# Kernel tuning notes

Hardware: AMD Instinct MI355X
Metric: run time of the kernel (lower is better)

## Reference

```python
import jax, jax.numpy as jnp
import numpy as np

FG_FRACTION = 0.5
FG_THRESH = 0.7
BG_HI = 0.5
BG_LO = 0.1
BATCHSIZE = 256
FG_ROIS = int(round(FG_FRACTION * BATCHSIZE))  # 128


def setup_inputs() -> dict:
    key = jax.random.key(0)
    k1, k2, k3 = jax.random.split(key, 3)
    N, K, C = 80000, 256, 81
    IMG = 800.0

    def make_boxes(k, n):
        ka, kb = jax.random.split(k)
        xy = jax.random.uniform(ka, (1, n, 2), dtype=jnp.float32) * (IMG - 136.0)
        wh = jax.random.uniform(kb, (1, n, 2), dtype=jnp.float32) * 128.0 + 8.0
        return jnp.concatenate([xy, xy + wh], axis=-1)  # valid x1<x2, y1<y2

    proposals = make_boxes(k1, N)          # (1, N, 4)
    gt_boxes = make_boxes(k2, K)           # (1, K, 4)
    cls = jax.random.randint(k3, (K,), 1, C)
    gt_labels = jax.nn.one_hot(cls, C, dtype=jnp.float32)[None]  # (1, K, C)
    return {"proposals": proposals, "gt_labels": gt_labels, "gt_boxes": gt_boxes}


def _iou(a, b):
    # a: (M,4), b: (K,4); keras_rcnn +1-pixel convention
    area_a = (a[:, 2] - a[:, 0] + 1.0) * (a[:, 3] - a[:, 1] + 1.0)
    area_b = (b[:, 2] - b[:, 0] + 1.0) * (b[:, 3] - b[:, 1] + 1.0)
    x1 = jnp.maximum(a[:, None, 0], b[None, :, 0])
    y1 = jnp.maximum(a[:, None, 1], b[None, :, 1])
    x2 = jnp.minimum(a[:, None, 2], b[None, :, 2])
    y2 = jnp.minimum(a[:, None, 3], b[None, :, 3])
    iw = jnp.maximum(x2 - x1 + 1.0, 0.0)
    ih = jnp.maximum(y2 - y1 + 1.0, 0.0)
    inter = iw * ih  # (M, K)
    return inter / (area_a[:, None] + area_b[None, :] - inter)


def _bbox_transform(ex, gt):
    ew = ex[:, 2] - ex[:, 0] + 1.0
    eh = ex[:, 3] - ex[:, 1] + 1.0
    ecx = ex[:, 0] + 0.5 * ew
    ecy = ex[:, 1] + 0.5 * eh
    gw = gt[:, 2] - gt[:, 0] + 1.0
    gh = gt[:, 3] - gt[:, 1] + 1.0
    gcx = gt[:, 0] + 0.5 * gw
    gcy = gt[:, 1] + 0.5 * gh
    return jnp.stack([(gcx - ecx) / ew, (gcy - ecy) / eh,
                      jnp.log(gw / ew), jnp.log(gh / eh)], axis=1)  # (B, 4)


def _forward(proposals, gt_labels, gt_boxes):
    all_rois = jnp.concatenate([proposals[0], gt_boxes[0]], axis=0)  # (M, 4)
    gt_b = gt_boxes[0]    # (K, 4)
    gt_l = gt_labels[0]   # (K, C)
    C = gt_l.shape[1]

    ov = _iou(all_rois, gt_b)               # (M, K)
    gt_assign = jnp.argmax(ov, axis=1)      # (M,)
    max_ov = jnp.max(ov, axis=1)            # (M,)

    fg_mask = max_ov >= FG_THRESH
    bg_mask = (max_ov < BG_HI) & (max_ov >= BG_LO)

    M = all_rois.shape[0]
    order = jnp.arange(M)
    # deterministic stand-in for random shuffle: candidates first, in index order
    fg_sorted = jnp.argsort(jnp.where(fg_mask, order, M + order))
    bg_sorted = jnp.argsort(jnp.where(bg_mask, order, M + order))
    num_fg = jnp.sum(fg_mask.astype(jnp.int32))
    fg_take = jnp.minimum(FG_ROIS, num_fg)

    pos = jnp.arange(BATCHSIZE)
    is_fg_slot = pos < fg_take
    keep = jnp.where(is_fg_slot,
                     fg_sorted[jnp.clip(pos, 0, M - 1)],
                     bg_sorted[jnp.clip(pos - fg_take, 0, M - 1)])  # (B,)

    rois = all_rois[keep]                    # (B, 4)
    labels = gt_l[gt_assign[keep]]           # (B, C)
    # set_label_background: bg slots -> one-hot class 0
    bg_onehot = jax.nn.one_hot(0, C, dtype=labels.dtype)
    labels = jnp.where(is_fg_slot[:, None], labels, bg_onehot[None, :])

    assigned_gt = gt_b[gt_assign[keep]]      # (B, 4)
    targets = _bbox_transform(rois, assigned_gt)  # (B, 4)

    # expand to N x 4K: only the argmax class (if > 0) gets nonzero targets
    clss = jnp.argmax(labels, axis=1)        # (B,)
    cls_oh = jnp.where((clss > 0)[:, None],
                       jax.nn.one_hot(clss, C, dtype=targets.dtype), 0.0)  # (B, C)
    bbox_targets = (cls_oh[:, :, None] * targets[:, None, :]).reshape(BATCHSIZE, 4 * C)

    return rois[None], labels[None], bbox_targets[None]


def reference(proposals, gt_labels, gt_boxes):
    return _forward(proposals, gt_labels, gt_boxes)
```

## Files before the change

kernel.cpp:

```cpp
#include <hip/hip_runtime.h>

#define FG_THRESH 0.7f
#define BG_HI 0.5f
#define BG_LO 0.1f
#define BATCH 256
#define FG_ROIS 128
#define KGT 256
#define CLS 81
#define NCHPAD2 1536
#define CPT2 3
#define NBIN 26
#define NSPAN 6

typedef unsigned long long ull;

__global__ __launch_bounds__(256) void k_iou(
    const float* __restrict__ proposals,
    const float* __restrict__ gt_boxes,
    int N, int M,
    int* __restrict__ gt_assign,
    ull* __restrict__ fgm,
    ull* __restrict__ bgm)
{
    __shared__ float4 gshE[KGT];
    __shared__ float garea[KGT];
    __shared__ ull pbx[4][NBIN], pby[4][NBIN];
    __shared__ ull intX[4][NBIN][NSPAN], intY[4][NBIN][NSPAN];

    int tid = threadIdx.x;
    int wv = tid >> 6, lane = tid & 63;

    float4 g = ((const float4*)gt_boxes)[tid];
    gshE[tid] = g;
    garea[tid] = (g.z - g.x + 1.0f) * (g.w - g.y + 1.0f);

    for (int b = 0; b < NBIN; ++b) {
        float hiE = 32.0f * (float)(b + 1);
        float loE = 32.0f * (float)b - 1.0f;
        ull mx = __ballot((g.x < hiE) && (g.z > loE));
        ull my = __ballot((g.y < hiE) && (g.w > loE));
        if (lane == 0) { pbx[wv][b] = mx; pby[wv][b] = my; }
    }
    __syncthreads();

    if (tid < 104) {
        int c = tid / NBIN, b = tid % NBIN;
        ull m = pbx[c][b];
        intX[c][b][0] = m;
        #pragma unroll
        for (int s = 1; s < NSPAN; ++s) {
            int bb = b + s;
            if (bb < NBIN) m |= pbx[c][bb];
            intX[c][b][s] = m;
        }
    } else if (tid >= 128 && tid < 232) {
        int u = tid - 128;
        int c = u / NBIN, b = u % NBIN;
        ull m = pby[c][b];
        intY[c][b][0] = m;
        #pragma unroll
        for (int s = 1; s < NSPAN; ++s) {
            int bb = b + s;
            if (bb < NBIN) m |= pby[c][bb];
            intY[c][b][s] = m;
        }
    }
    __syncthreads();

    int c = lane & 3;
    int rj = lane >> 2;
    int ch = blockIdx.x;
    int roi = ch * 64 + wv * 16 + rj;
    bool val = (roi < M);

    float4 a;
    if (val) a = (roi < N) ? ((const float4*)proposals)[roi] : gshE[roi - N];
    else     a = gshE[0];
    float az1 = a.z + 1.0f, aw1 = a.w + 1.0f;
    float area_a = (a.z - a.x + 1.0f) * (a.w - a.y + 1.0f);

    int b1x = (int)(a.x * 0.03125f);
    int b2x = min((int)(az1 * 0.03125f), NBIN - 1);
    int b1y = (int)(a.y * 0.03125f);
    int b2y = min((int)(aw1 * 0.03125f), NBIN - 1);
    int sx = b2x - b1x;
    int sy = b2y - b1y;

    ull mbits = val ? (intX[c][b1x][sx] & intY[c][b1y][sy]) : 0ull;

    float best = 0.0f;
    int bestk = 0;
    while (mbits) {
        int j = __ffsll(mbits) - 1;
        mbits &= mbits - 1;
        int k = (c << 6) + j;
        float4 gg = gshE[k];
        float x1 = fmaxf(a.x, gg.x);
        float y1 = fmaxf(a.y, gg.y);
        float x2 = fminf(a.z, gg.z);
        float y2 = fminf(a.w, gg.w);
        float iw = fmaxf(x2 - x1 + 1.0f, 0.0f);
        float ih = fmaxf(y2 - y1 + 1.0f, 0.0f);
        float inter = iw * ih;
        float q = inter / (area_a + garea[k] - inter);
        if (q > best) { best = q; bestk = k; }
    }

    #pragma unroll
    for (int d = 1; d < 4; d <<= 1) {
        float ob = __shfl_xor(best, d);
        int   kb = __shfl_xor(bestk, d);
        if (ob > best || (ob == best && kb < bestk)) { best = ob; bestk = kb; }
    }
    float bset = __shfl(best, (lane & 15) * 4);
    int   bk   = __shfl(bestk, (lane & 15) * 4);

    int roi2 = ch * 64 + wv * 16 + (lane & 15);
    bool isv = (lane < 16) && (roi2 < M);
    bool fgp = isv && (bset >= FG_THRESH);
    bool bgp = isv && (bset < BG_HI) && (bset >= BG_LO);
    if (isv) gt_assign[roi2] = bk;

    ull mf = __ballot(fgp);
    ull mb = __ballot(bgp);
    if (lane == 0) {
        ((unsigned short*)fgm)[(ch << 2) | wv] = (unsigned short)mf;
        ((unsigned short*)bgm)[(ch << 2) | wv] = (unsigned short)mb;
    }
}

__global__ __launch_bounds__(512) void k_finish(
    const float* __restrict__ proposals,
    const float* __restrict__ gt_boxes,
    const float* __restrict__ gt_labels,
    int N, int NCH,
    const int* __restrict__ gt_assign,
    const ull* __restrict__ fgm,
    const ull* __restrict__ bgm,
    float* __restrict__ out_rois,
    float* __restrict__ out_labels,
    float4* __restrict__ out_bbox)
{
    __shared__ ull sf[NCHPAD2], sb[NCHPAD2];
    __shared__ int pf[NCHPAD2], pb[NCHPAD2], pn[NCHPAD2];
    __shared__ int fgl[FG_ROIS], bgl[BATCH], nbl[BATCH];
    __shared__ int wtot[3][8];
    __shared__ int lm_cls[8];
    __shared__ float4 lm_t[8];

    int tid = threadIdx.x;
    int lane = tid & 63, wv = tid >> 6;
    int lo = tid * CPT2;

    ull wf[CPT2], wb[CPT2];
    int vmsk[CPT2];
    #pragma unroll
    for (int r = 0; r < CPT2; ++r) {
        int idx = lo + r;
        bool v = (idx < NCH);
        vmsk[r] = v;
        wf[r] = v ? fgm[idx] : 0ull;
        wb[r] = v ? bgm[idx] : 0ull;
    }
    int pc0 = 0, pc1 = 0, pc2 = 0;
    #pragma unroll
    for (int r = 0; r < CPT2; ++r) {
        pc0 += __popcll(wf[r]);
        pc1 += __popcll(wb[r]);
        pc2 += vmsk[r] ? __popcll(~wb[r]) : 0;
    }

    int i0 = pc0, i1 = pc1, i2 = pc2;
    #pragma unroll
    for (int d = 1; d < 64; d <<= 1) {
        int t0 = __shfl_up(i0, d);
        int t1 = __shfl_up(i1, d);
        int t2 = __shfl_up(i2, d);
        if (lane >= d) { i0 += t0; i1 += t1; i2 += t2; }
    }
    if (lane == 63) { wtot[0][wv] = i0; wtot[1][wv] = i1; wtot[2][wv] = i2; }
    __syncthreads();
    int o0 = 0, o1 = 0, o2 = 0;
    for (int x = 0; x < wv; ++x) { o0 += wtot[0][x]; o1 += wtot[1][x]; o2 += wtot[2][x]; }
    int b0 = o0 + i0 - pc0;
    int b1 = o1 + i1 - pc1;
    int b2 = o2 + i2 - pc2;
    int num_fg = 0, num_bg = 0;
    #pragma unroll
    for (int x = 0; x < 8; ++x) { num_fg += wtot[0][x]; num_bg += wtot[1][x]; }
    int fg_take = min(FG_ROIS, num_fg);
    bool need_nb = (fg_take + num_bg < BATCH);

    #pragma unroll
    for (int r = 0; r < CPT2; ++r) {
        int w = lo + r;
        sf[w] = wf[r];
        sb[w] = wb[r];
        pf[w] = b0; b0 += __popcll(wf[r]);
        pb[w] = b1; b1 += __popcll(wb[r]);
        pn[w] = b2; b2 += vmsk[r] ? __popcll(~wb[r]) : 0;
    }
    __syncthreads();

    #pragma unroll
    for (int pass = 0; pass < CPT2; ++pass) {
        int w = tid + 512 * pass;
        int base = pf[w];
        if (base < FG_ROIS) {
            ull m = sf[w];
            while (m) {
                if (base >= FG_ROIS) break;
                fgl[base++] = (w << 6) + __ffsll(m) - 1;
                m &= m - 1;
            }
        }
        base = pb[w];
        if (base < BATCH) {
            ull m = sb[w];
            while (m) {
                if (base >= BATCH) break;
                bgl[base++] = (w << 6) + __ffsll(m) - 1;
                m &= m - 1;
            }
        }
        if (need_nb) {
            base = pn[w];
            if (base < BATCH) {
                ull m = (w < NCH) ? ~sb[w] : 0ull;
                while (m) {
                    if (base >= BATCH) break;
                    nbl[base++] = (w << 6) + __ffsll(m) - 1;
                    m &= m - 1;
                }
            }
        }
    }
    __syncthreads();

    int eBase = blockIdx.x * 512;
    int posLo = eBase / CLS;
    int posHi = min((eBase + 511) / CLS, BATCH - 1);
    int np = posHi - posLo + 1;

    if (wv < np) {
        int pos = posLo + wv;
        int is_fg = (pos < fg_take) ? 1 : 0;
        int j = pos - fg_take;
        int keep = is_fg ? fgl[pos] : ((j < num_bg) ? bgl[j] : nbl[j - num_bg]);
        float4 a = (keep < N) ? ((const float4*)proposals)[keep]
                              : ((const float4*)gt_boxes)[keep - N];
        int ga = gt_assign[keep];
        float4 g = ((const float4*)gt_boxes)[ga];

        float ew = a.z - a.x + 1.0f, eh = a.w - a.y + 1.0f;
        float ecx = a.x + 0.5f * ew, ecy = a.y + 0.5f * eh;
        float gw = g.z - g.x + 1.0f, gh = g.w - g.y + 1.0f;
        float gcx = g.x + 0.5f * gw, gcy = g.y + 0.5f * gh;

        int cls = 0;
        if (is_fg) {
            float l1 = gt_labels[(size_t)ga * CLS + lane];
            int c2 = lane + 64;
            float l2 = (c2 < CLS) ? gt_labels[(size_t)ga * CLS + c2] : 0.0f;
            ull m1 = __ballot(l1 > 0.5f);
            ull m2 = __ballot(c2 < CLS && l2 > 0.5f);
            cls = m1 ? (__ffsll(m1) - 1) : (m2 ? 64 + __ffsll(m2) - 1 : 0);
        }
        if (lane == 0) {
            lm_cls[wv] = cls;
            lm_t[wv] = make_float4((gcx - ecx) / ew, (gcy - ecy) / eh,
                                   logf(gw / ew), logf(gh / eh));
        }
    }

    if (blockIdx.x == 0 && tid < BATCH) {
        int pos = tid;
        int is_fg = (pos < fg_take) ? 1 : 0;
        int j = pos - fg_take;
        int keep = is_fg ? fgl[pos] : ((j < num_bg) ? bgl[j] : nbl[j - num_bg]);
        float4 a = (keep < N) ? ((const float4*)proposals)[keep]
                              : ((const float4*)gt_boxes)[keep - N];
        ((float4*)out_rois)[pos] = a;
    }
    __syncthreads();

    int e = eBase + tid;
    if (e < BATCH * CLS) {
        int pos = e / CLS, cc = e - pos * CLS;
        int li = pos - posLo;
        int cl = lm_cls[li];
        out_labels[e] = (cc == cl) ? 1.0f : 0.0f;
        out_bbox[e] = (cl > 0 && cc == cl) ? lm_t[li]
                                           : make_float4(0.f, 0.f, 0.f, 0.f);
    }
}

extern "C" void kernel_launch(void* const* d_in, const int* in_sizes, int n_in,
                              void* d_out, int out_size, void* d_ws, size_t ws_size,
                              hipStream_t stream)
{
    const float* proposals = (const float*)d_in[0];
    const float* gt_labels = (const float*)d_in[1];
    const float* gt_boxes  = (const float*)d_in[2];
    int N = in_sizes[0] / 4;
    int K = in_sizes[2] / 4;
    int M = N + K;
    int NCH = (M + 63) / 64;

    char* ws = (char*)d_ws;
    size_t off = 0;
    auto alloc = [&](size_t bytes) -> void* {
        void* p = ws + off;
        off += (bytes + 255) & ~(size_t)255;
        return p;
    };
    int* gt_assign = (int*)alloc((size_t)M * 4);
    ull* fgm = (ull*)alloc((size_t)NCH * 8);
    ull* bgm = (ull*)alloc((size_t)NCH * 8);

    float* out_rois   = (float*)d_out;
    float* out_labels = out_rois + BATCH * 4;
    float4* out_bbox  = (float4*)(out_labels + BATCH * CLS);

    k_iou<<<NCH, 256, 0, stream>>>(proposals, gt_boxes, N, M,
                                   gt_assign, fgm, bgm);
    int nb2 = (BATCH * CLS + 511) / 512;
    k_finish<<<nb2, 512, 0, stream>>>(proposals, gt_boxes, gt_labels, N, NCH,
                                      gt_assign, fgm, bgm,
                                      out_rois, out_labels, out_bbox);
    (void)K; (void)n_in; (void)out_size; (void)ws_size;
}
```

Measured before the change: 23.56 us.

## Split finish kernel so background-only blocks skip mask compaction

```diff
diff --git a/kernel.cpp b/kernel.cpp
--- a/kernel.cpp
+++ b/kernel.cpp
@@ -141,6 +141,7 @@
     float* __restrict__ out_labels,
     float4* __restrict__ out_bbox)
 {
+    __shared__ float4 gshE[KGT];
     __shared__ ull sf[NCHPAD2], sb[NCHPAD2];
     __shared__ int pf[NCHPAD2], pb[NCHPAD2], pn[NCHPAD2];
     __shared__ int fgl[FG_ROIS], bgl[BATCH], nbl[BATCH];
@@ -150,24 +151,40 @@
 
     int tid = threadIdx.x;
     int lane = tid & 63, wv = tid >> 6;
+    int nOut = (int)gridDim.x - 1;
+    bool isRois = ((int)blockIdx.x == nOut);
+    int eBase = blockIdx.x * 512;
+    int posLo = eBase / CLS;
+
+    if (!isRois && posLo >= FG_ROIS) {
+        int e = eBase + tid;
+        if (e < BATCH * CLS) {
+            int pos = e / CLS, cc = e - pos * CLS;
+            out_labels[e] = (cc == 0) ? 1.0f : 0.0f;
+            out_bbox[e] = make_float4(0.f, 0.f, 0.f, 0.f);
+        }
+        return;
+    }
+
+    if (tid < KGT) gshE[tid] = ((const float4*)gt_boxes)[tid];
+
     int lo = tid * CPT2;
-
     ull wf[CPT2], wb[CPT2];
-    int vmsk[CPT2];
+    int vm[CPT2];
     #pragma unroll
     for (int r = 0; r < CPT2; ++r) {
         int idx = lo + r;
         bool v = (idx < NCH);
-        vmsk[r] = v;
+        vm[r] = v;
         wf[r] = v ? fgm[idx] : 0ull;
-        wb[r] = v ? bgm[idx] : 0ull;
+        wb[r] = (isRois && v) ? bgm[idx] : 0ull;
     }
     int pc0 = 0, pc1 = 0, pc2 = 0;
     #pragma unroll
     for (int r = 0; r < CPT2; ++r) {
         pc0 += __popcll(wf[r]);
         pc1 += __popcll(wb[r]);
-        pc2 += vmsk[r] ? __popcll(~wb[r]) : 0;
+        pc2 += vm[r] ? __popcll(~wb[r]) : 0;
     }
 
     int i0 = pc0, i1 = pc1, i2 = pc2;
@@ -195,10 +212,12 @@
     for (int r = 0; r < CPT2; ++r) {
         int w = lo + r;
         sf[w] = wf[r];
-        sb[w] = wb[r];
         pf[w] = b0; b0 += __popcll(wf[r]);
-        pb[w] = b1; b1 += __popcll(wb[r]);
-        pn[w] = b2; b2 += vmsk[r] ? __popcll(~wb[r]) : 0;
+        if (isRois) {
+            sb[w] = wb[r];
+            pb[w] = b1; b1 += __popcll(wb[r]);
+            pn[w] = b2; b2 += vm[r] ? __popcll(~wb[r]) : 0;
+        }
     }
     __syncthreads();
 
@@ -214,73 +233,76 @@
                 m &= m - 1;
             }
         }
-        base = pb[w];
-        if (base < BATCH) {
-            ull m = sb[w];
-            while (m) {
-                if (base >= BATCH) break;
-                bgl[base++] = (w << 6) + __ffsll(m) - 1;
-                m &= m - 1;
-            }
-        }
-        if (need_nb) {
-            base = pn[w];
+        if (isRois) {
+            base = pb[w];
             if (base < BATCH) {
-                ull m = (w < NCH) ? ~sb[w] : 0ull;
+                ull m = sb[w];
                 while (m) {
                     if (base >= BATCH) break;
-                    nbl[base++] = (w << 6) + __ffsll(m) - 1;
+                    bgl[base++] = (w << 6) + __ffsll(m) - 1;
                     m &= m - 1;
                 }
             }
-        }
-    }
-    __syncthreads();
-
-    int eBase = blockIdx.x * 512;
-    int posLo = eBase / CLS;
+            if (need_nb) {
+                base = pn[w];
+                if (base < BATCH) {
+                    ull m = (w < NCH) ? ~sb[w] : 0ull;
+                    while (m) {
+                        if (base >= BATCH) break;
+                        nbl[base++] = (w << 6) + __ffsll(m) - 1;
+                        m &= m - 1;
+                    }
+                }
+            }
+        }
+    }
+    __syncthreads();
+
+    if (isRois) {
+        if (tid < BATCH) {
+            int pos = tid;
+            int is_fg = (pos < fg_take) ? 1 : 0;
+            int j = pos - fg_take;
+            int keep = is_fg ? fgl[pos] : ((j < num_bg) ? bgl[j] : nbl[j - num_bg]);
+            float4 a = (keep < N) ? ((const float4*)proposals)[keep]
+                                  : gshE[keep - N];
+            ((float4*)out_rois)[pos] = a;
+        }
+        return;
+    }
+
     int posHi = min((eBase + 511) / CLS, BATCH - 1);
     int np = posHi - posLo + 1;
 
     if (wv < np) {
         int pos = posLo + wv;
-        int is_fg = (pos < fg_take) ? 1 : 0;
-        int j = pos - fg_take;
-        int keep = is_fg ? fgl[pos] : ((j < num_bg) ? bgl[j] : nbl[j - num_bg]);
-        float4 a = (keep < N) ? ((const float4*)proposals)[keep]
-                              : ((const float4*)gt_boxes)[keep - N];
-        int ga = gt_assign[keep];
-        float4 g = ((const float4*)gt_boxes)[ga];
-
-        float ew = a.z - a.x + 1.0f, eh = a.w - a.y + 1.0f;
-        float ecx = a.x + 0.5f * ew, ecy = a.y + 0.5f * eh;
-        float gw = g.z - g.x + 1.0f, gh = g.w - g.y + 1.0f;
-        float gcx = g.x + 0.5f * gw, gcy = g.y + 0.5f * gh;
-
-        int cls = 0;
-        if (is_fg) {
+        if (pos < fg_take) {
+            int keep = fgl[pos];
+            float4 a = (keep < N) ? ((const float4*)proposals)[keep]
+                                  : gshE[keep - N];
+            int ga = gt_assign[keep];
+            float4 g = gshE[ga];
+
+            float ew = a.z - a.x + 1.0f, eh = a.w - a.y + 1.0f;
+            float ecx = a.x + 0.5f * ew, ecy = a.y + 0.5f * eh;
+            float gw = g.z - g.x + 1.0f, gh = g.w - g.y + 1.0f;
+            float gcx = g.x + 0.5f * gw, gcy = g.y + 0.5f * gh;
+
             float l1 = gt_labels[(size_t)ga * CLS + lane];
             int c2 = lane + 64;
             float l2 = (c2 < CLS) ? gt_labels[(size_t)ga * CLS + c2] : 0.0f;
             ull m1 = __ballot(l1 > 0.5f);
             ull m2 = __ballot(c2 < CLS && l2 > 0.5f);
-            cls = m1 ? (__ffsll(m1) - 1) : (m2 ? 64 + __ffsll(m2) - 1 : 0);
-        }
-        if (lane == 0) {
-            lm_cls[wv] = cls;
-            lm_t[wv] = make_float4((gcx - ecx) / ew, (gcy - ecy) / eh,
-                                   logf(gw / ew), logf(gh / eh));
-        }
-    }
-
-    if (blockIdx.x == 0 && tid < BATCH) {
-        int pos = tid;
-        int is_fg = (pos < fg_take) ? 1 : 0;
-        int j = pos - fg_take;
-        int keep = is_fg ? fgl[pos] : ((j < num_bg) ? bgl[j] : nbl[j - num_bg]);
-        float4 a = (keep < N) ? ((const float4*)proposals)[keep]
-                              : ((const float4*)gt_boxes)[keep - N];
-        ((float4*)out_rois)[pos] = a;
+            int cls = m1 ? (__ffsll(m1) - 1) : (m2 ? 64 + __ffsll(m2) - 1 : 0);
+
+            if (lane == 0) {
+                lm_cls[wv] = cls;
+                lm_t[wv] = make_float4((gcx - ecx) / ew, (gcy - ecy) / eh,
+                                       logf(gw / ew), logf(gh / eh));
+            }
+        } else {
+            if (lane == 0) lm_cls[wv] = 0;
+        }
     }
     __syncthreads();
 
@@ -324,7 +346,7 @@
 
     k_iou<<<NCH, 256, 0, stream>>>(proposals, gt_boxes, N, M,
                                    gt_assign, fgm, bgm);
-    int nb2 = (BATCH * CLS + 511) / 512;
+    int nb2 = (BATCH * CLS + 511) / 512 + 1;
     k_finish<<<nb2, 512, 0, stream>>>(proposals, gt_boxes, gt_labels, N, NCH,
                                       gt_assign, fgm, bgm,
                                       out_rois, out_labels, out_bbox);
```

Measured after the change: 22.19 us, median of 2. -5.8%, faster.
